# Performance work log

Hardware: AMD Instinct MI355X
Metric: run time of the kernel (lower is better)

Reference implementation:

```python
import jax, jax.numpy as jnp
import numpy as np

N = 100000
E = 1600000
D_IN, D_HID, D_OUT = 256, 256, 128


def _sage_conv(x, src, dst, Wl, bl, Wr, n_nodes):
    # PyG SAGEConv (aggr='mean'): out = lin_l(mean_{j in N(i)} x_j) + lin_r(x_i)
    msg = x[src]                                               # [E, d]
    summed = jax.ops.segment_sum(msg, dst, num_segments=n_nodes)  # [N, d]
    deg = jax.ops.segment_sum(jnp.ones((src.shape[0],), x.dtype), dst,
                              num_segments=n_nodes)            # [N]
    agg = summed / jnp.maximum(deg, 1.0)[:, None]              # mean, 0 if isolated
    return agg @ Wl.T + bl + x @ Wr.T


def setup_inputs() -> dict:
    key = jax.random.key(0)
    ks = jax.random.split(key, 8)
    x = jax.random.normal(ks[0], (N, D_IN), dtype=jnp.float32)
    edge_index = jax.random.randint(ks[1], (2, E), 0, N, dtype=jnp.int32)
    s1 = 1.0 / np.sqrt(D_IN)
    s2 = 1.0 / np.sqrt(D_HID)
    W1l = jax.random.uniform(ks[2], (D_HID, D_IN), jnp.float32, -s1, s1)
    b1 = jnp.zeros((D_HID,), jnp.float32)
    W1r = jax.random.uniform(ks[3], (D_HID, D_IN), jnp.float32, -s1, s1)
    W2l = jax.random.uniform(ks[4], (D_OUT, D_HID), jnp.float32, -s2, s2)
    b2 = jnp.zeros((D_OUT,), jnp.float32)
    W2r = jax.random.uniform(ks[5], (D_OUT, D_HID), jnp.float32, -s2, s2)
    return {"x": x, "edge_index": edge_index, "W1l": W1l, "b1": b1,
            "W1r": W1r, "W2l": W2l, "b2": b2, "W2r": W2r}


def reference(x, edge_index, W1l, b1, W1r, W2l, b2, W2r):
    src, dst = edge_index[0], edge_index[1]
    h = _sage_conv(x, src, dst, W1l, b1, W1r, x.shape[0])
    h = jax.nn.relu(h)
    out = _sage_conv(h, src, dst, W2l, b2, W2r, x.shape[0])
    return out
```

## Files before the change

kernel.cpp:

```cpp
#include <hip/hip_runtime.h>

#define DK 256
#define BN 256
#define NBLK 512

typedef __attribute__((ext_vector_type(8))) short bf16x8;
typedef __attribute__((ext_vector_type(4))) float f32x4;

__device__ __forceinline__ unsigned short f2b(float f) {
    unsigned u = __builtin_bit_cast(unsigned, f);
    u += 0x7FFFu + ((u >> 16) & 1u);
    return (unsigned short)(u >> 16);
}
__device__ __forceinline__ float b2f(unsigned short s) {
    return __builtin_bit_cast(float, (unsigned)s << 16);
}
__device__ __forceinline__ void gld_lds16(void* lds, const void* g) {
    __builtin_amdgcn_global_load_lds(
        (const __attribute__((address_space(1))) unsigned int*)g,
        (__attribute__((address_space(3))) unsigned int*)lds, 16, 0, 0);
}

__global__ __launch_bounds__(256) void k_cvt(const float* __restrict__ src,
                                             unsigned short* __restrict__ dst, int n4) {
    int i = blockIdx.x * 256 + threadIdx.x;
    if (i < n4) {
        float4 v = reinterpret_cast<const float4*>(src)[i];
        ushort4 o = make_ushort4(f2b(v.x), f2b(v.y), f2b(v.z), f2b(v.w));
        reinterpret_cast<ushort4*>(dst)[i] = o;
    }
}

__global__ __launch_bounds__(256) void k_cvtw(const float* __restrict__ a,
                                              const float* __restrict__ b,
                                              const float* __restrict__ c,
                                              const float* __restrict__ d,
                                              unsigned short* __restrict__ Wb1,
                                              unsigned short* __restrict__ Wb2) {
    int i = blockIdx.x * 256 + threadIdx.x;
    const float* s;
    unsigned short* o;
    if (i < 16384)      { s = a; o = Wb1; }
    else if (i < 32768) { s = b; o = Wb1 + 256 * 256; i -= 16384; }
    else if (i < 40960) { s = c; o = Wb2;             i -= 32768; }
    else                { s = d; o = Wb2 + 128 * 256; i -= 40960; }
    float4 v = reinterpret_cast<const float4*>(s)[i];
    ushort4 w = make_ushort4(f2b(v.x), f2b(v.y), f2b(v.z), f2b(v.w));
    reinterpret_cast<ushort4*>(o)[i] = w;
}

__global__ __launch_bounds__(256) void k_scan_a(const int* __restrict__ in,
                                                int* __restrict__ bsum, int N) {
    __shared__ int sm[256];
    int t = threadIdx.x;
    int i0 = blockIdx.x * 1024 + t * 4;
    int s = 0;
    if (i0 + 3 < N) {
        int4 v = *reinterpret_cast<const int4*>(in + i0);
        s = v.x + v.y + v.z + v.w;
    } else {
        for (int i = i0; i < min(i0 + 4, N); ++i) s += in[i];
    }
    sm[t] = s;
    __syncthreads();
    for (int off = 128; off > 0; off >>= 1) {
        if (t < off) sm[t] += sm[t + off];
        __syncthreads();
    }
    if (t == 0) bsum[blockIdx.x] = sm[0];
}

__global__ __launch_bounds__(256) void k_scan_b(const int* __restrict__ bsum,
                                                int* __restrict__ boff,
                                                int* __restrict__ totN, int NB) {
    __shared__ int sm[256];
    int t = threadIdx.x;
    sm[t] = (t < NB) ? bsum[t] : 0;
    __syncthreads();
    for (int off = 1; off < 256; off <<= 1) {
        int v = (t >= off) ? sm[t - off] : 0;
        __syncthreads();
        sm[t] += v;
        __syncthreads();
    }
    if (t < NB) boff[t] = (t == 0) ? 0 : sm[t - 1];
    if (t == NB - 1) *totN = sm[t];
}

__global__ __launch_bounds__(256) void k_scan_c2(const int* __restrict__ in,
                                                 const int* __restrict__ boff,
                                                 int* __restrict__ outx, int N) {
    __shared__ int sm[256];
    int t = threadIdx.x;
    int i0 = blockIdx.x * 1024 + t * 4;
    int d0 = 0, d1 = 0, d2 = 0, d3 = 0;
    if (i0 + 3 < N) {
        int4 v = *reinterpret_cast<const int4*>(in + i0);
        d0 = v.x; d1 = v.y; d2 = v.z; d3 = v.w;
    } else {
        if (i0 + 0 < N) d0 = in[i0 + 0];
        if (i0 + 1 < N) d1 = in[i0 + 1];
        if (i0 + 2 < N) d2 = in[i0 + 2];
        if (i0 + 3 < N) d3 = in[i0 + 3];
    }
    int s = d0 + d1 + d2 + d3;
    sm[t] = s;
    __syncthreads();
    for (int off = 1; off < 256; off <<= 1) {
        int v = (t >= off) ? sm[t - off] : 0;
        __syncthreads();
        sm[t] += v;
        __syncthreads();
    }
    int run = boff[blockIdx.x] + sm[t] - s;
    int dd[4] = {d0, d1, d2, d3};
#pragma unroll
    for (int i = 0; i < 4; ++i) {
        int idx = i0 + i;
        if (idx < N) { outx[idx] = run; run += dd[i]; }
    }
}

__global__ __launch_bounds__(256) void k_hist(const int* __restrict__ dst,
                                              int* __restrict__ hist,
                                              int E, int NBUK) {
    extern __shared__ int h[];
    int t = threadIdx.x;
    for (int b = t; b < NBUK; b += 256) h[b] = 0;
    __syncthreads();
    int CH = (E + NBLK - 1) / NBLK;
    int beg = blockIdx.x * CH;
    int end = min(beg + CH, E);
    for (int i = beg + t; i < end; i += 256)
        atomicAdd(&h[dst[i] >> 8], 1);
    __syncthreads();
    for (int b = t; b < NBUK; b += 256)
        hist[b * NBLK + blockIdx.x] = h[b];
}

__global__ __launch_bounds__(256) void k_part(const int* __restrict__ src,
                                              const int* __restrict__ dst,
                                              const int* __restrict__ hoff,
                                              unsigned* __restrict__ scratch,
                                              int E, int NBUK) {
    extern __shared__ int cur[];
    int t = threadIdx.x;
    for (int b = t; b < NBUK; b += 256) cur[b] = hoff[b * NBLK + blockIdx.x];
    __syncthreads();
    int CH = (E + NBLK - 1) / NBLK;
    int beg = blockIdx.x * CH;
    int end = min(beg + CH, E);
    for (int i = beg + t; i < end; i += 256) {
        int d = dst[i];
        int p = atomicAdd(&cur[d >> 8], 1);
        scratch[p] = (unsigned)src[i] | ((unsigned)(d & 255) << 20);
    }
}

__global__ __launch_bounds__(256) void k_scatter3(const unsigned* __restrict__ scratch,
                                                  const int* __restrict__ hoff,
                                                  int* __restrict__ rowptr,
                                                  float* __restrict__ invdeg,
                                                  int* __restrict__ col,
                                                  int E, int NBUK, int N) {
    __shared__ int cnt[BN];
    __shared__ int sm[256];
    __shared__ int cur[BN];
    int b = blockIdx.x, t = threadIdx.x;
    cnt[t] = 0;
    __syncthreads();
    int beg = hoff[b * NBLK];
    int end = (b + 1 < NBUK) ? hoff[(b + 1) * NBLK] : E;
    for (int i = beg + t; i < end; i += 256)
        atomicAdd(&cnt[scratch[i] >> 20], 1);
    __syncthreads();
    int v = cnt[t];
    sm[t] = v;
    __syncthreads();
    for (int off = 1; off < 256; off <<= 1) {
        int u = (t >= off) ? sm[t - off] : 0;
        __syncthreads();
        sm[t] += u;
        __syncthreads();
    }
    int node = b * BN + t;
    if (node < N) {
        int start = beg + sm[t] - v;
        rowptr[node] = start;
        cur[t] = start;
        invdeg[node] = 1.0f / fmaxf((float)v, 1.0f);
    }
    if (b == 0 && t == 0) rowptr[N] = E;
    __syncthreads();
    for (int i = beg + t; i < end; i += 256) {
        unsigned s = scratch[i];
        int p = atomicAdd(&cur[s >> 20], 1);
        col[p] = (int)(s & 0xFFFFFu);
    }
}

template <bool RF32, int NT>
__global__ __launch_bounds__(256) void k_gemm_bf16(const unsigned short* __restrict__ A,
                                                   const unsigned short* __restrict__ W,
                                                   unsigned short* __restrict__ Y,
                                                   void* __restrict__ Rv, int N) {
    constexpr int DOUTA = NT * 64;
    __shared__ unsigned short As[128 * 32];
    __shared__ unsigned short Bs[128 * 32];
    const int tid  = threadIdx.x;
    const int lane = tid & 63;
    const int w    = tid >> 6;
    const int wm   = w & 1, wn = w >> 1;
    const int m0   = blockIdx.x * 128;
    const int lm   = lane & 15, quad = lane >> 4;

    const int srow  = lane >> 2;
    const int skoff = (lane & 3) * 8;
    const int ca = 2 * w, cb = 2 * w + 1;

    for (int nt = 0; nt < NT; ++nt) {
        const int n0 = nt * 128;
        f32x4 acc[4][4];
#pragma unroll
        for (int i = 0; i < 4; ++i)
#pragma unroll
            for (int j = 0; j < 4; ++j) acc[i][j] = (f32x4){0.f, 0.f, 0.f, 0.f};

        for (int k0 = 0; k0 < DK; k0 += 32) {
            int ra = min(m0 + 16 * ca + srow, N - 1);
            int rb = min(m0 + 16 * cb + srow, N - 1);
            gld_lds16(As + ca * 512, A + (size_t)ra * DK + k0 + skoff);
            gld_lds16(As + cb * 512, A + (size_t)rb * DK + k0 + skoff);
            int na = n0 + 16 * ca + srow;
            int nb = n0 + 16 * cb + srow;
            gld_lds16(Bs + ca * 512, W + (size_t)na * DK + k0 + skoff);
            gld_lds16(Bs + cb * 512, W + (size_t)nb * DK + k0 + skoff);
            __syncthreads();

            bf16x8 af[4], bfr[4];
#pragma unroll
            for (int mt = 0; mt < 4; ++mt)
                af[mt] = *reinterpret_cast<const bf16x8*>(As + (wm * 64 + mt * 16 + lm) * 32 + quad * 8);
#pragma unroll
            for (int ntf = 0; ntf < 4; ++ntf)
                bfr[ntf] = *reinterpret_cast<const bf16x8*>(Bs + (wn * 64 + ntf * 16 + lm) * 32 + quad * 8);
#pragma unroll
            for (int mt = 0; mt < 4; ++mt)
#pragma unroll
                for (int ntf = 0; ntf < 4; ++ntf)
                    acc[mt][ntf] = __builtin_amdgcn_mfma_f32_16x16x32_bf16(af[mt], bfr[ntf], acc[mt][ntf], 0, 0, 0);
            __syncthreads();
        }

        const bool yPart = (n0 < DOUTA);
#pragma unroll
        for (int mt = 0; mt < 4; ++mt) {
#pragma unroll
            for (int ntf = 0; ntf < 4; ++ntf) {
                int gn = n0 + wn * 64 + ntf * 16 + lm;
#pragma unroll
                for (int reg = 0; reg < 4; ++reg) {
                    int gm = m0 + wm * 64 + mt * 16 + quad * 4 + reg;
                    if (gm < N) {
                        float v = acc[mt][ntf][reg];
                        if (yPart) {
                            Y[(size_t)gm * DOUTA + gn] = f2b(v);
                        } else if (RF32) {
                            ((float*)Rv)[(size_t)gm * DOUTA + (gn - DOUTA)] = v;
                        } else {
                            ((unsigned short*)Rv)[(size_t)gm * DOUTA + (gn - DOUTA)] = f2b(v);
                        }
                    }
                }
            }
        }
    }
}

__global__ __launch_bounds__(256) void k_agg256(const unsigned short* __restrict__ Y,
                                                const unsigned short* __restrict__ Rb,
                                                const float* __restrict__ bias,
                                                const float* __restrict__ invdeg,
                                                const int* __restrict__ rowptr,
                                                const int* __restrict__ col,
                                                unsigned short* __restrict__ H, int N) {
    int g = blockIdx.x * 256 + threadIdx.x;
    int node = g >> 6;
    int lane = g & 63;
    if (node >= N) return;
    int half = lane >> 5, sub = lane & 31;
    int beg = rowptr[node], end = rowptr[node + 1];
    const unsigned short* yb = Y + sub * 8;
    float a[8];
#pragma unroll
    for (int j = 0; j < 8; ++j) a[j] = 0.f;
    int e = beg;
    for (; e + 7 < end; e += 8) {
        int s[4];
#pragma unroll
        for (int u = 0; u < 4; ++u) s[u] = col[e + 2 * u + half];
        bf16x8 v[4];
#pragma unroll
        for (int u = 0; u < 4; ++u)
            v[u] = *reinterpret_cast<const bf16x8*>(yb + (size_t)s[u] * 256);
#pragma unroll
        for (int u = 0; u < 4; ++u)
#pragma unroll
            for (int j = 0; j < 8; ++j) a[j] += b2f((unsigned short)v[u][j]);
    }
    for (; e + 1 < end; e += 2) {
        int s0 = col[e + half];
        bf16x8 v0 = *reinterpret_cast<const bf16x8*>(yb + (size_t)s0 * 256);
#pragma unroll
        for (int j = 0; j < 8; ++j) a[j] += b2f((unsigned short)v0[j]);
    }
    if (e < end && half == 0) {
        int s0 = col[e];
        bf16x8 v0 = *reinterpret_cast<const bf16x8*>(yb + (size_t)s0 * 256);
#pragma unroll
        for (int j = 0; j < 8; ++j) a[j] += b2f((unsigned short)v0[j]);
    }
#pragma unroll
    for (int j = 0; j < 8; ++j) a[j] += __shfl_xor(a[j], 32);
    if (half == 0) {
        float inv = invdeg[node];
        int c = sub * 8;
        bf16x8 r = *reinterpret_cast<const bf16x8*>(Rb + (size_t)node * 256 + c);
        f32x4 b0 = *reinterpret_cast<const f32x4*>(bias + c);
        f32x4 b1v = *reinterpret_cast<const f32x4*>(bias + c + 4);
        bf16x8 o;
#pragma unroll
        for (int j = 0; j < 8; ++j) {
            float bj = (j < 4) ? b0[j] : b1v[j - 4];
            float ov = fmaxf(a[j] * inv + bj + b2f((unsigned short)r[j]), 0.f);
            o[j] = (short)f2b(ov);
        }
        *reinterpret_cast<bf16x8*>(H + (size_t)node * 256 + c) = o;
    }
}

__global__ __launch_bounds__(256) void k_agg128(const unsigned short* __restrict__ Y,
                                                const float* __restrict__ Rf,
                                                const float* __restrict__ bias,
                                                const float* __restrict__ invdeg,
                                                const int* __restrict__ rowptr,
                                                const int* __restrict__ col,
                                                float* __restrict__ O, int N) {
    int g = blockIdx.x * 256 + threadIdx.x;
    int node = g >> 6;
    int lane = g & 63;
    if (node >= N) return;
    int half = lane >> 5, sub = lane & 31;
    int beg = rowptr[node], end = rowptr[node + 1];
    const unsigned short* yb = Y + sub * 4;
    float a0 = 0, a1 = 0, a2 = 0, a3 = 0;
    int e = beg;
    for (; e + 7 < end; e += 8) {
        int s[4];
#pragma unroll
        for (int u = 0; u < 4; ++u) s[u] = col[e + 2 * u + half];
        ushort4 v[4];
#pragma unroll
        for (int u = 0; u < 4; ++u)
            v[u] = *reinterpret_cast<const ushort4*>(yb + (size_t)s[u] * 128);
#pragma unroll
        for (int u = 0; u < 4; ++u) {
            a0 += b2f(v[u].x); a1 += b2f(v[u].y);
            a2 += b2f(v[u].z); a3 += b2f(v[u].w);
        }
    }
    for (; e + 1 < end; e += 2) {
        int s0 = col[e + half];
        ushort4 v0 = *reinterpret_cast<const ushort4*>(yb + (size_t)s0 * 128);
        a0 += b2f(v0.x); a1 += b2f(v0.y); a2 += b2f(v0.z); a3 += b2f(v0.w);
    }
    if (e < end && half == 0) {
        int s0 = col[e];
        ushort4 v0 = *reinterpret_cast<const ushort4*>(yb + (size_t)s0 * 128);
        a0 += b2f(v0.x); a1 += b2f(v0.y); a2 += b2f(v0.z); a3 += b2f(v0.w);
    }
    a0 += __shfl_xor(a0, 32);
    a1 += __shfl_xor(a1, 32);
    a2 += __shfl_xor(a2, 32);
    a3 += __shfl_xor(a3, 32);
    if (half == 0) {
        float inv = invdeg[node];
        int c = sub * 4;
        f32x4 r = *reinterpret_cast<const f32x4*>(Rf + (size_t)node * 128 + c);
        f32x4 bv = *reinterpret_cast<const f32x4*>(bias + c);
        f32x4 o;
        o[0] = a0 * inv + bv[0] + r[0];
        o[1] = a1 * inv + bv[1] + r[1];
        o[2] = a2 * inv + bv[2] + r[2];
        o[3] = a3 * inv + bv[3] + r[3];
        *reinterpret_cast<f32x4*>(O + (size_t)node * 128 + c) = o;
    }
}

extern "C" void kernel_launch(void* const* d_in, const int* in_sizes, int n_in,
                              void* d_out, int out_size, void* d_ws, size_t ws_size,
                              hipStream_t stream) {
    const float* x   = (const float*)d_in[0];
    const int*   ei  = (const int*)d_in[1];
    const float* W1l = (const float*)d_in[2];
    const float* b1  = (const float*)d_in[3];
    const float* W1r = (const float*)d_in[4];
    const float* W2l = (const float*)d_in[5];
    const float* b2  = (const float*)d_in[6];
    const float* W2r = (const float*)d_in[7];
    float* out = (float*)d_out;

    const int N = in_sizes[0] / DK;
    const int E = in_sizes[1] / 2;
    const int* src = ei;
    const int* dst = ei + E;

    unsigned short* xb  = (unsigned short*)d_ws;
    unsigned short* y1b = xb + (size_t)N * 256;
    unsigned short* r1b = y1b + (size_t)N * 256;
    unsigned short* hb  = r1b + (size_t)N * 256;
    unsigned short* Wb1 = hb + (size_t)N * 256;
    unsigned short* Wb2 = Wb1 + 512 * 256;
    float* invdeg = (float*)(Wb2 + 256 * 256);
    int* rowptr = (int*)(invdeg + N);
    int* col    = rowptr + (N + 1);
    int* bsum   = col + E;
    int* boff   = bsum + 512;
    unsigned short* y2b = y1b;
    float* r2f = (float*)r1b;

    const int NBUK = (N + BN - 1) / BN;
    const int NH   = NBUK * NBLK;
    unsigned* scratch = (unsigned*)hb;
    int* hist  = (int*)y1b;
    int* hoff  = hist + NH;
    int* tot2  = boff + 512;

    k_cvt<<<(N * 64 + 255) / 256, 256, 0, stream>>>(x, xb, N * 64);
    k_cvtw<<<192, 256, 0, stream>>>(W1l, W1r, W2l, W2r, Wb1, Wb2);

    const int NB2 = (NH + 1023) / 1024;
    k_hist<<<NBLK, 256, NBUK * sizeof(int), stream>>>(dst, hist, E, NBUK);
    k_scan_a<<<NB2, 256, 0, stream>>>(hist, bsum, NH);
    k_scan_b<<<1, 256, 0, stream>>>(bsum, boff, tot2, NB2);
    k_scan_c2<<<NB2, 256, 0, stream>>>(hist, boff, hoff, NH);
    k_part<<<NBLK, 256, NBUK * sizeof(int), stream>>>(src, dst, hoff, scratch, E, NBUK);
    k_scatter3<<<NBUK, 256, 0, stream>>>(scratch, hoff, rowptr, invdeg, col, E, NBUK, N);

    int mTiles = (N + 127) / 128;
    int aggBlocks = (N + 3) / 4;

    k_gemm_bf16<false, 4><<<mTiles, 256, 0, stream>>>(xb, Wb1, y1b, r1b, N);
    k_agg256<<<aggBlocks, 256, 0, stream>>>(y1b, r1b, b1, invdeg, rowptr, col, hb, N);

    k_gemm_bf16<true, 2><<<mTiles, 256, 0, stream>>>(hb, Wb2, y2b, r2f, N);
    k_agg128<<<aggBlocks, 256, 0, stream>>>(y2b, r2f, b2, invdeg, rowptr, col, out, N);
}
```

Measured before the change: 533.5 us.

## Double GEMM K-tile to 64 and XOR-swizzle LDS layout

The bf16 GEMM kernel now stages 64-wide K slices of A and W in LDS instead of 32, halving the number of barrier pairs per output tile. The LDS layout applies an XOR swizzle on 16-byte chunks so that the fragment reads, now at a 128-byte row stride, avoid bank conflicts. In exchange LDS use per block doubles, which may lower occupancy, and the swizzle adds some index arithmetic.

```diff
diff --git a/kernel.cpp b/kernel.cpp
--- a/kernel.cpp
+++ b/kernel.cpp
@@ -205,8 +205,8 @@
                                                    unsigned short* __restrict__ Y,
                                                    void* __restrict__ Rv, int N) {
     constexpr int DOUTA = NT * 64;
-    __shared__ unsigned short As[128 * 32];
-    __shared__ unsigned short Bs[128 * 32];
+    __shared__ unsigned short As[128 * 64];
+    __shared__ unsigned short Bs[128 * 64];
     const int tid  = threadIdx.x;
     const int lane = tid & 63;
     const int w    = tid >> 6;
@@ -214,9 +214,9 @@
     const int m0   = blockIdx.x * 128;
     const int lm   = lane & 15, quad = lane >> 4;
 
-    const int srow  = lane >> 2;
-    const int skoff = (lane & 3) * 8;
-    const int ca = 2 * w, cb = 2 * w + 1;
+    const int srow = lane >> 3;
+    const int sko  = ((lane & 7) ^ srow) * 8;
+    const int rsw  = lm & 7;
 
     for (int nt = 0; nt < NT; ++nt) {
         const int n0 = nt * 128;
@@ -226,29 +226,36 @@
 #pragma unroll
             for (int j = 0; j < 4; ++j) acc[i][j] = (f32x4){0.f, 0.f, 0.f, 0.f};
 
-        for (int k0 = 0; k0 < DK; k0 += 32) {
-            int ra = min(m0 + 16 * ca + srow, N - 1);
-            int rb = min(m0 + 16 * cb + srow, N - 1);
-            gld_lds16(As + ca * 512, A + (size_t)ra * DK + k0 + skoff);
-            gld_lds16(As + cb * 512, A + (size_t)rb * DK + k0 + skoff);
-            int na = n0 + 16 * ca + srow;
-            int nb = n0 + 16 * cb + srow;
-            gld_lds16(Bs + ca * 512, W + (size_t)na * DK + k0 + skoff);
-            gld_lds16(Bs + cb * 512, W + (size_t)nb * DK + k0 + skoff);
+        for (int k0 = 0; k0 < DK; k0 += 64) {
+#pragma unroll
+            for (int c = 0; c < 4; ++c) {
+                int ch = 4 * w + c;
+                int ra = min(m0 + ch * 8 + srow, N - 1);
+                gld_lds16(As + ch * 512, A + (size_t)ra * DK + k0 + sko);
+                int na = n0 + ch * 8 + srow;
+                gld_lds16(Bs + ch * 512, W + (size_t)na * DK + k0 + sko);
+            }
             __syncthreads();
 
-            bf16x8 af[4], bfr[4];
-#pragma unroll
-            for (int mt = 0; mt < 4; ++mt)
-                af[mt] = *reinterpret_cast<const bf16x8*>(As + (wm * 64 + mt * 16 + lm) * 32 + quad * 8);
-#pragma unroll
-            for (int ntf = 0; ntf < 4; ++ntf)
-                bfr[ntf] = *reinterpret_cast<const bf16x8*>(Bs + (wn * 64 + ntf * 16 + lm) * 32 + quad * 8);
-#pragma unroll
-            for (int mt = 0; mt < 4; ++mt)
+#pragma unroll
+            for (int kk = 0; kk < 2; ++kk) {
+                const int xo = (quad ^ (kk * 4) ^ rsw) * 8;
+                bf16x8 af[4], bfr[4];
+#pragma unroll
+                for (int mt = 0; mt < 4; ++mt)
+                    af[mt] = *reinterpret_cast<const bf16x8*>(
+                        As + (wm * 64 + mt * 16 + lm) * 64 + xo);
 #pragma unroll
                 for (int ntf = 0; ntf < 4; ++ntf)
-                    acc[mt][ntf] = __builtin_amdgcn_mfma_f32_16x16x32_bf16(af[mt], bfr[ntf], acc[mt][ntf], 0, 0, 0);
+                    bfr[ntf] = *reinterpret_cast<const bf16x8*>(
+                        Bs + (wn * 64 + ntf * 16 + lm) * 64 + xo);
+#pragma unroll
+                for (int mt = 0; mt < 4; ++mt)
+#pragma unroll
+                    for (int ntf = 0; ntf < 4; ++ntf)
+                        acc[mt][ntf] = __builtin_amdgcn_mfma_f32_16x16x32_bf16(
+                            af[mt], bfr[ntf], acc[mt][ntf], 0, 0, 0);
+            }
             __syncthreads();
         }
 
```

New measurement: 525.8 us. No clear change (-1.5%).
